# Kernel tuning notes

Hardware: AMD Instinct MI355X
Metric: run time of the kernel (lower is better)

The kernel has to match this reference:

```python
import math
import jax, jax.numpy as jnp
import numpy as np

B, N, D_IN = 8, 4096, 512  # batch, tokens (64x64 grid), d_inner = expand*d_model
MAX_DIFFUSION = 0.35
ALPHA_SCALE = 0.25
BETA_EPS = 1e-4


def setup_inputs() -> dict:
    key = jax.random.key(0)
    ks = jax.random.split(key, 6)
    x = jax.random.normal(ks[0], (B, N, D_IN), dtype=jnp.float32)
    # diffusion_gate: Linear(d_inner, d_inner) with tiny uniform init and softplus-inv(0.08) bias
    Wg = jax.random.uniform(ks[1], (D_IN, D_IN), jnp.float32, -1e-4, 1e-4)
    bg = jnp.full((D_IN,), math.log(math.exp(0.08) - 1.0), dtype=jnp.float32)
    log_base = jnp.full((1, D_IN), -2.5, dtype=jnp.float32)
    alpha_raw = 0.1 * jax.random.normal(ks[2], (1, 1, D_IN), dtype=jnp.float32)
    beta_raw = jnp.full((1, 1, D_IN), -2.0, dtype=jnp.float32)
    # out_complex: Linear(2*d_inner, d_inner, bias=False); torch weight shape [out, in]
    Wout = jax.random.normal(ks[3], (D_IN, 2 * D_IN), jnp.float32) / math.sqrt(2 * D_IN)
    Dparam = jnp.ones((D_IN,), dtype=jnp.float32)
    return {"x": x, "Wg": Wg, "bg": bg, "log_base": log_base,
            "alpha_raw": alpha_raw, "beta_raw": beta_raw,
            "Wout": Wout, "Dparam": Dparam, "k_steps": 4}


def _reaction(psi, alpha, beta, dt):
    # Exact update of q=|psi|^2 under dq/dt = 2*alpha*q - 2*beta*q^2; phase unchanged.
    eps = 1e-8
    q = jnp.real(psi) ** 2 + jnp.imag(psi) ** 2
    a = 2.0 * alpha
    b = 2.0 * beta
    exp_term = jnp.exp(-a * dt)
    denom = jnp.maximum(b * q + (a - b * q) * exp_term, eps)
    q_general = a * q / denom
    q_zero_alpha = q / (1.0 + b * q * dt)
    q_new = jnp.maximum(jnp.where(jnp.abs(a) < 1e-6, q_zero_alpha, q_general), 0.0)
    scale = jnp.sqrt(q_new / jnp.maximum(q, eps))
    return psi * scale


def reference(x, Wg, bg, log_base, alpha_raw, beta_raw, Wout, Dparam, k_steps):
    bsz, num_tokens, d_inner = x.shape
    h = w = int(math.isqrt(num_tokens))
    pooled = x.mean(axis=1)                                   # [B, d]
    gamma = jax.nn.softplus(pooled @ Wg.T + bg + log_base)    # [B, d]
    gamma = jnp.minimum(gamma, MAX_DIFFUSION).astype(jnp.float32)
    alpha = (ALPHA_SCALE * jnp.tanh(alpha_raw)).transpose(0, 2, 1)[..., None]   # [1, d, 1, 1]
    beta = (jax.nn.softplus(beta_raw) + BETA_EPS).transpose(0, 2, 1)[..., None]  # [1, d, 1, 1]
    # Periodic 2D Laplacian eigenvalues
    ky = jnp.arange(h, dtype=jnp.float32)
    kx = jnp.arange(w, dtype=jnp.float32)
    eig = (2.0 * jnp.cos(2.0 * jnp.pi * ky / h) - 2.0)[:, None] + \
          (2.0 * jnp.cos(2.0 * jnp.pi * kx / w) - 2.0)[None, :]  # [h, w]
    dt = 1.0 / max(int(k_steps), 1)
    psi = x.transpose(0, 2, 1).reshape(bsz, d_inner, h, w).astype(jnp.complex64)
    phase_arg = dt * gamma[:, :, None, None] * eig[None, None, :, :]  # [B, d, h, w]
    phase = jnp.cos(phase_arg) + 1j * jnp.sin(phase_arg)
    for _ in range(int(k_steps)):
        psi = _reaction(psi, alpha, beta, 0.5 * dt)
        psi = jnp.fft.ifft2(jnp.fft.fft2(psi, axes=(-2, -1)) * phase, axes=(-2, -1))
        psi = _reaction(psi, alpha, beta, 0.5 * dt)
    h_real = jnp.real(psi).reshape(bsz, d_inner, num_tokens).transpose(0, 2, 1)
    h_imag = jnp.imag(psi).reshape(bsz, d_inner, num_tokens).transpose(0, 2, 1)
    combined = jnp.concatenate([h_real, h_imag], axis=-1).astype(x.dtype)  # [B, N, 2d]
    return combined @ Wout.T + x * Dparam
```

## Files before the change

### kernel.cpp

```cpp
#include <hip/hip_runtime.h>
#include <math.h>


#define D_INNER 512
#define NTOK    4096

typedef _Float16 half8 __attribute__((ext_vector_type(8)));
typedef float    f32x4 __attribute__((ext_vector_type(4)));

struct cplx { float re, im; };

__device__ __forceinline__ cplx cmul(cplx a, cplx b) {
  return { a.re * b.re - a.im * b.im, a.re * b.im + a.im * b.re };
}

template<int CTRL>
__device__ __forceinline__ float dppf(float x) {
  return __int_as_float(__builtin_amdgcn_mov_dpp(__float_as_int(x), CTRL, 0xf, 0xf, true));
}
#define DPP_XOR1 0xB1
#define DPP_XOR2 0x4E

template<int SIGN>
__device__ __forceinline__ void fft16(cplx* a) {
  const float C16[8] = {1.f, 0.9238795325112867f, 0.7071067811865476f, 0.3826834323650898f,
                        0.f, -0.3826834323650898f, -0.7071067811865476f, -0.9238795325112867f};
  const float S16[8] = {0.f, 0.3826834323650898f, 0.7071067811865476f, 0.9238795325112867f,
                        1.f, 0.9238795325112867f, 0.7071067811865476f, 0.3826834323650898f};
  cplx t;
#define SWP(i, j) { t = a[i]; a[i] = a[j]; a[j] = t; }
  SWP(1, 8) SWP(2, 4) SWP(3, 12) SWP(5, 10) SWP(7, 14) SWP(11, 13)
#undef SWP
#pragma unroll
  for (int s = 1; s <= 4; ++s) {
    const int half = 1 << (s - 1);
#pragma unroll
    for (int base = 0; base < 16; base += (1 << s)) {
#pragma unroll
      for (int j = 0; j < (1 << (s - 1)); ++j) {
        const int ti = j << (4 - s);
        const float wc = C16[ti];
        const float ws = (SIGN < 0) ? -S16[ti] : S16[ti];
        cplx u = a[base + j];
        cplx v = a[base + j + half];
        cplx vw = { v.re * wc - v.im * ws, v.re * ws + v.im * wc };
        a[base + j]        = { u.re + vw.re, u.im + vw.im };
        a[base + j + half] = { u.re - vw.re, u.im - vw.im };
      }
    }
  }
}

__device__ __forceinline__ cplx fwd_cross(cplx z, bool s1, bool s2) {
  cplx w;  w.re = dppf<DPP_XOR2>(z.re);  w.im = dppf<DPP_XOR2>(z.im);
  cplx z1;
  z1.re = s2 ? (w.re - z.re) : (z.re + w.re);
  z1.im = s2 ? (w.im - z.im) : (z.im + w.im);
  cplx w2; w2.re = dppf<DPP_XOR1>(z1.re); w2.im = dppf<DPP_XOR1>(z1.im);
  cplx o;
  o.re = s1 ? (w2.re - (s2 ? z1.im : z1.re))
            : (z1.re + (s2 ? w2.im : w2.re));
  o.im = s1 ? (w2.im + (s2 ? z1.re : -z1.im))
            : (z1.im + (s2 ? -w2.re : w2.im));
  return o;
}

__device__ __forceinline__ cplx inv_cross(cplx z, bool s1, bool s2) {
  cplx w;  w.re = dppf<DPP_XOR1>(z.re);  w.im = dppf<DPP_XOR1>(z.im);
  cplx z1;
  z1.re = s1 ? (w.re - z.re) : (z.re + w.re);
  z1.im = s1 ? (w.im - z.im) : (z.im + w.im);
  cplx w2; w2.re = dppf<DPP_XOR2>(z1.re); w2.im = dppf<DPP_XOR2>(z1.im);
  cplx o;
  o.re = s2 ? (w2.re + (s1 ? z1.im : -z1.re))
            : (z1.re + (s1 ? -w2.im : w2.re));
  o.im = s2 ? (w2.im - (s1 ? z1.re : z1.im))
            : (z1.im + (s1 ? w2.re : w2.im));
  return o;
}

template<int SIGN>
__device__ __forceinline__ void fft64(cplx* a, bool s1, bool s2,
                                      const float* twc, const float* tws) {
  if (SIGN < 0) {
#pragma unroll
    for (int i = 0; i < 16; ++i) a[i] = fwd_cross(a[i], s1, s2);
#pragma unroll
    for (int i = 0; i < 16; ++i) {
      float c = twc[i], s = tws[i];
      cplx v = a[i];
      a[i] = { v.re * c + v.im * s, v.im * c - v.re * s };
    }
    fft16<-1>(a);
  } else {
    fft16<1>(a);
#pragma unroll
    for (int i = 0; i < 16; ++i) {
      float c = twc[i], s = tws[i];
      cplx v = a[i];
      a[i] = { v.re * c - v.im * s, v.im * c + v.re * s };
    }
#pragma unroll
    for (int i = 0; i < 16; ++i) a[i] = inv_cross(a[i], s1, s2);
  }
}

__device__ __forceinline__ void reaction_fast(cplx* a, float sA, float cB, float cC) {
#pragma unroll
  for (int i = 0; i < 16; ++i) {
    float q = fmaf(a[i].re, a[i].re, a[i].im * a[i].im);
    float s = sA * rsqrtf(fmaf(cB, q, cC));
    a[i].re *= s; a[i].im *= s;
  }
}


__global__ void zero_kernel(float* p, int n) {
  int i = blockIdx.x * blockDim.x + threadIdx.x;
  if (i < n) p[i] = 0.f;
}

__global__ __launch_bounds__(256) void transpose_pool_kernel(
    const float* __restrict__ x, float* __restrict__ xT, float* __restrict__ pooled) {
  __shared__ float tile[64][65];
  const int n0 = blockIdx.x * 64, d0 = blockIdx.y * 64, b = blockIdx.z;
  const int t = threadIdx.x;
  const int tc = t & 63, tr = t >> 6;
  const float* xp = x + ((size_t)b * NTOK + n0) * D_INNER + d0;
#pragma unroll
  for (int i = 0; i < 16; ++i) {
    int nl = tr + i * 4;
    tile[nl][tc] = xp[(size_t)nl * D_INNER + tc];
  }
  __syncthreads();
  float* xo = xT + ((size_t)b * D_INNER + d0) * NTOK + n0;
#pragma unroll
  for (int i = 0; i < 16; ++i) {
    int dl = tr + i * 4;
    xo[(size_t)dl * NTOK + tc] = tile[tc][dl];
  }
  if (t < 64) {
    float s = 0.f;
#pragma unroll
    for (int n = 0; n < 64; ++n) s += tile[n][t];
    atomicAdd(&pooled[b * D_INNER + d0 + t], s);
  }
}

__global__ __launch_bounds__(256) void gamma_kernel(
    const float* __restrict__ pooled, const float* __restrict__ Wg,
    const float* __restrict__ bg, const float* __restrict__ log_base,
    float* __restrict__ gamma) {
  int t = blockIdx.x * 256 + threadIdx.x;
  int b = t >> 9, j = t & 511;
  const float* pr = pooled + b * D_INNER;
  const float* wr = Wg + (size_t)j * D_INNER;
  float acc = 0.f;
#pragma unroll 4
  for (int d = 0; d < D_INNER; ++d) acc = fmaf(pr[d], wr[d], acc);
  float z = acc * (1.f / 4096.f) + bg[j] + log_base[j];
  float sp = fmaxf(z, 0.f) + log1pf(expf(-fabsf(z)));
  gamma[t] = fminf(sp, 0.35f);
}

__global__ __launch_bounds__(256) void plane_kernel(
    const float* __restrict__ xT, const float* __restrict__ gamma,
    const float* __restrict__ alpha_raw, const float* __restrict__ beta_raw,
    const int* __restrict__ kstep_p, _Float16* __restrict__ S) {
  __shared__ float2 T[64 * 65];
  __shared__ float2 P[64];
  const int blk = blockIdx.x;
  const int bb = blk >> 9, d = blk & 511;
  const int tid = threadIdx.x;
  const int lb = tid & 3;
  const int rr = tid >> 2;
  const bool s1 = lb & 1, s2 = (lb & 2) != 0;

  int ks = kstep_p[0]; if (ks < 1) ks = 1;
  const float dt  = 1.0f / (float)ks;
  const float dtr = 0.5f * dt;
  const float a2 = 2.0f * 0.25f * tanhf(alpha_raw[d]);
  float zb = beta_raw[d];
  const float b2 = 2.0f * (fmaxf(zb, 0.f) + log1pf(expf(-fabsf(zb))) + 1e-4f);

  _Float16* Sre = S + ((size_t)(bb * 1024 + d)) * NTOK + rr * 64 + lb * 16;
  _Float16* Sim = S + ((size_t)(bb * 1024 + 512 + d)) * NTOK + rr * 64 + lb * 16;

  if (a2 <= -1e-6f) {
    half8 z = {};
    *(half8*)&Sre[0] = z; *(half8*)&Sre[8] = z;
    *(half8*)&Sim[0] = z; *(half8*)&Sim[8] = z;
    return;
  }

  float sA, cB, cC;
  if (a2 < 1e-6f) {
    sA = 1.f; cB = b2 * dtr; cC = 1.f;
  } else {
    float ex = expf(-a2 * dtr);
    sA = sqrtf(a2); cB = b2 * (1.f - ex); cC = a2 * ex;
  }
  const float cg = dt * gamma[(bb << 9) + d];

  const float TWO_PI_64 = 6.283185307179586f / 64.0f;
  if (tid < 64) {
    float e = 2.0f * cosf(TWO_PI_64 * (float)tid) - 2.0f;
    float sv, cv; sincosf(cg * e, &sv, &cv);
    P[tid] = make_float2(cv * 0.015625f, sv * 0.015625f);
  }
  const int k2 = (lb == 1) ? 2 : ((lb == 2) ? 1 : lb);
  float twc[16], tws[16];
  {
    float c1, s1v; sincosf(TWO_PI_64 * (float)k2, &s1v, &c1);
    twc[0] = 1.f; tws[0] = 0.f;
#pragma unroll
    for (int i = 1; i < 16; ++i) {
      float pc = twc[i-1], ps = tws[i-1];
      twc[i] = pc * c1 - ps * s1v;
      tws[i] = ps * c1 + pc * s1v;
    }
  }

  cplx a[16];
  const float* px = xT + (size_t)blk * NTOK + rr * 64 + lb * 16;
#pragma unroll
  for (int i = 0; i < 4; ++i) {
    float4 v = *(const float4*)(px + i * 4);
    a[i*4+0] = { v.x, 0.f }; a[i*4+1] = { v.y, 0.f };
    a[i*4+2] = { v.z, 0.f }; a[i*4+3] = { v.w, 0.f };
  }
  __syncthreads();

  for (int step = 0; step < ks; ++step) {
    reaction_fast(a, sA, cB, cC);
    fft64<-1>(a, s1, s2, twc, tws);
    __syncthreads();
#pragma unroll
    for (int i = 0; i < 16; ++i)
      T[rr * 65 + (k2 + 4 * i)] = make_float2(a[i].re, a[i].im);
    __syncthreads();
#pragma unroll
    for (int i = 0; i < 16; ++i) {
      float2 v = T[(lb * 16 + i) * 65 + rr];
      a[i] = { v.x, v.y };
    }
    fft64<-1>(a, s1, s2, twc, tws);
    {
      float2 pc = P[rr];
      cplx pcc = { pc.x, pc.y };
#pragma unroll
      for (int i = 0; i < 16; ++i) {
        float2 pk = P[k2 + 4 * i];
        a[i] = cmul(a[i], cmul({pk.x, pk.y}, pcc));
      }
    }
    fft64<1>(a, s1, s2, twc, tws);
    __syncthreads();
#pragma unroll
    for (int i = 0; i < 16; ++i)
      T[(lb * 16 + i) * 65 + rr] = make_float2(a[i].re, a[i].im);
    __syncthreads();
#pragma unroll
    for (int i = 0; i < 16; ++i) {
      float2 v = T[rr * 65 + (k2 + 4 * i)];
      a[i] = { v.x, v.y };
    }
    fft64<1>(a, s1, s2, twc, tws);
    reaction_fast(a, sA, cB, cC);
  }

  half8 hr0, hr1, hi0, hi1;
#pragma unroll
  for (int i = 0; i < 8; ++i) {
    hr0[i] = (_Float16)a[i].re;     hi0[i] = (_Float16)a[i].im;
    hr1[i] = (_Float16)a[8+i].re;   hi1[i] = (_Float16)a[8+i].im;
  }
  *(half8*)&Sre[0] = hr0; *(half8*)&Sre[8] = hr1;
  *(half8*)&Sim[0] = hi0; *(half8*)&Sim[8] = hi1;
}

__global__ __launch_bounds__(256) void transpose_S_kernel(
    const _Float16* __restrict__ S, _Float16* __restrict__ ST) {
  __shared__ __attribute__((aligned(16))) _Float16 tile[64 * 64];
  const int n0 = blockIdx.x * 64, k0 = blockIdx.y * 64, b = blockIdx.z;
  const int t = threadIdx.x;
#pragma unroll
  for (int r = 0; r < 2; ++r) {
    int idx = r * 256 + t, kr = idx >> 3, c = idx & 7;
    half8 v = *(const half8*)&S[((size_t)b * 1024 + k0 + kr) * NTOK + n0 + c * 8];
    *(half8*)&tile[kr * 64 + ((c ^ (kr & 7)) * 8)] = v;
  }
  __syncthreads();
#pragma unroll
  for (int r = 0; r < 2; ++r) {
    int idx = r * 256 + t, nr = idx >> 3, ck = idx & 7;
    half8 v;
#pragma unroll
    for (int j = 0; j < 8; ++j) {
      int k = ck * 8 + j;
      v[j] = tile[k * 64 + (((nr >> 3) ^ (k & 7)) * 8) + (nr & 7)];
    }
    *(half8*)&ST[((size_t)b * NTOK + n0 + nr) * 1024 + k0 + ck * 8] = v;
  }
}

__global__ __launch_bounds__(256) void out_gemm_f16(
    const _Float16* __restrict__ ST, const float* __restrict__ Wout,
    const float* __restrict__ x, const float* __restrict__ Dp,
    float* __restrict__ out) {
  __shared__ __attribute__((aligned(16))) _Float16 Abuf[2][128 * 32];
  __shared__ __attribute__((aligned(16))) _Float16 Bbuf[2][128 * 32];
  const int t = threadIdx.x;
  const int n0 = blockIdx.x * 128, j0 = blockIdx.y * 128, b = blockIdx.z;
  const int w = t >> 6, l = t & 63;
  const int jw = (w & 1) * 64, nw = (w >> 1) * 64;
  const int l15 = l & 15, l4 = l >> 4;

  const int sr = t >> 1, skh = t & 1;
  const int br_ = t >> 2, bc = t & 3;
  const _Float16* Sb = ST + (size_t)b * NTOK * 1024;

  float aReg[16];
  half8 bReg0, bReg1;

  auto loadA = [&](int k0) {
    const float* src = Wout + (size_t)(j0 + sr) * 1024 + k0 + skh * 16;
    *(float4*)&aReg[0]  = *(const float4*)&src[0];
    *(float4*)&aReg[4]  = *(const float4*)&src[4];
    *(float4*)&aReg[8]  = *(const float4*)&src[8];
    *(float4*)&aReg[12] = *(const float4*)&src[12];
  };
  auto loadB = [&](int k0) {
    bReg0 = *(const half8*)&Sb[(size_t)(n0 + br_) * 1024 + k0 + bc * 8];
    bReg1 = *(const half8*)&Sb[(size_t)(n0 + 64 + br_) * 1024 + k0 + bc * 8];
  };
  auto writeA = [&](int buf) {
    half8 h0, h1;
#pragma unroll
    for (int i = 0; i < 8; ++i) { h0[i] = (_Float16)aReg[i]; h1[i] = (_Float16)aReg[8 + i]; }
    int c0 = skh * 2, c1 = skh * 2 + 1, s = (sr >> 1) & 3;
    *(half8*)&Abuf[buf][sr * 32 + ((c0 ^ s) * 8)] = h0;
    *(half8*)&Abuf[buf][sr * 32 + ((c1 ^ s) * 8)] = h1;
  };
  auto writeB = [&](int buf) {
    int r0 = br_, r1 = 64 + br_;
    *(half8*)&Bbuf[buf][r0 * 32 + ((bc ^ ((r0 >> 1) & 3)) * 8)] = bReg0;
    *(half8*)&Bbuf[buf][r1 * 32 + ((bc ^ ((r1 >> 1) & 3)) * 8)] = bReg1;
  };

  f32x4 acc[4][4] = {};
  loadA(0); loadB(0);
  writeA(0); writeB(0);
  __syncthreads();
  int cur = 0;
  for (int kt = 0; kt < 32; ++kt) {
    if (kt + 1 < 32) { loadA((kt + 1) * 32); loadB((kt + 1) * 32); }
    half8 af[4], bf[4];
#pragma unroll
    for (int ff = 0; ff < 4; ++ff) {
      int jr = jw + ff * 16 + l15;
      af[ff] = *(const half8*)&Abuf[cur][jr * 32 + (((l4 ^ (jr >> 1)) & 3) * 8)];
      int nr = nw + ff * 16 + l15;
      bf[ff] = *(const half8*)&Bbuf[cur][nr * 32 + (((l4 ^ (nr >> 1)) & 3) * 8)];
    }
#pragma unroll
    for (int jf = 0; jf < 4; ++jf)
#pragma unroll
      for (int nf = 0; nf < 4; ++nf)
        acc[jf][nf] = __builtin_amdgcn_mfma_f32_16x16x32_f16(af[jf], bf[nf], acc[jf][nf], 0, 0, 0);
    if (kt + 1 < 32) {
      cur ^= 1;
      writeA(cur); writeB(cur);
      __syncthreads();
    }
  }

#pragma unroll
  for (int jf = 0; jf < 4; ++jf) {
#pragma unroll
    for (int nf = 0; nf < 4; ++nf) {
      int jr4 = j0 + jw + jf * 16 + l4 * 4;
      int n   = n0 + nw + nf * 16 + l15;
      const float* xrow = x + ((size_t)b * NTOK + n) * D_INNER + jr4;
      float* orow = out + ((size_t)b * NTOK + n) * D_INNER + jr4;
      float4 xv = *(const float4*)xrow;
      float4 dv = *(const float4*)&Dp[jr4];
      float4 o;
      o.x = acc[jf][nf][0] + xv.x * dv.x;
      o.y = acc[jf][nf][1] + xv.y * dv.y;
      o.z = acc[jf][nf][2] + xv.z * dv.z;
      o.w = acc[jf][nf][3] + xv.w * dv.w;
      *(float4*)orow = o;
    }
  }
}


extern "C" void kernel_launch(void* const* d_in, const int* in_sizes, int n_in,
                              void* d_out, int out_size, void* d_ws, size_t ws_size,
                              hipStream_t stream) {
  const float* x         = (const float*)d_in[0];
  const float* Wg        = (const float*)d_in[1];
  const float* bg        = (const float*)d_in[2];
  const float* log_base  = (const float*)d_in[3];
  const float* alpha_raw = (const float*)d_in[4];
  const float* beta_raw  = (const float*)d_in[5];
  const float* Wout      = (const float*)d_in[6];
  const float* Dparam    = (const float*)d_in[7];
  const int*   kstep     = (const int*)d_in[8];
  float* out = (float*)d_out;

  char* ws = (char*)d_ws;
  float*    xT = (float*)ws;
  _Float16* S  = (_Float16*)(ws + 67108864);
  _Float16* STr = (_Float16*)ws;
  float* pooled = (float*)(ws + 134217728);
  float* gamma  = pooled + 8 * D_INNER;

  zero_kernel<<<16, 256, 0, stream>>>(pooled, 8 * D_INNER);
  transpose_pool_kernel<<<dim3(64, 8, 8), 256, 0, stream>>>(x, xT, pooled);
  gamma_kernel<<<16, 256, 0, stream>>>(pooled, Wg, bg, log_base, gamma);
  plane_kernel<<<4096, 256, 0, stream>>>(xT, gamma, alpha_raw, beta_raw, kstep, S);
  transpose_S_kernel<<<dim3(64, 16, 8), 256, 0, stream>>>(S, STr);
  out_gemm_f16<<<dim3(32, 4, 8), 256, 0, stream>>>(STr, Wout, x, Dparam, out);
}
```

Measured before the change: 505.3 us.

## Vectorize FFT math, merge reaction half-steps, pre-convert Wout, use global_load_lds

Rewrites the plane kernel's complex arithmetic with packed float2 vectors and branch-free cross-lane butterflies. Adjacent reaction half-steps are merged into one full-step update. A launch-bounds occupancy hint is added. Wout is converted to fp16 once in a separate kernel, and the GEMM stages A and B tiles straight into LDS with global_load_lds instead of going through registers; this drops the XOR swizzle, so LDS bank conflicts may rise.

Result: faster. 457.4 us (-9.5%).

```diff
diff --git a/kernel.cpp b/kernel.cpp
--- a/kernel.cpp
+++ b/kernel.cpp
@@ -7,27 +7,38 @@
 
 typedef _Float16 half8 __attribute__((ext_vector_type(8)));
 typedef float    f32x4 __attribute__((ext_vector_type(4)));
-
-struct cplx { float re, im; };
-
-__device__ __forceinline__ cplx cmul(cplx a, cplx b) {
-  return { a.re * b.re - a.im * b.im, a.re * b.im + a.im * b.re };
-}
+typedef float    f32x2 __attribute__((ext_vector_type(2)));
+
+#define DPP_XOR1 0xB1
+#define DPP_XOR2 0x4E
 
 template<int CTRL>
 __device__ __forceinline__ float dppf(float x) {
   return __int_as_float(__builtin_amdgcn_mov_dpp(__float_as_int(x), CTRL, 0xf, 0xf, true));
 }
-#define DPP_XOR1 0xB1
-#define DPP_XOR2 0x4E
+template<int CTRL>
+__device__ __forceinline__ f32x2 dpp2(f32x2 v) {
+  f32x2 r;
+  r.x = dppf<CTRL>(v.x);
+  r.y = dppf<CTRL>(v.y);
+  return r;
+}
+__device__ __forceinline__ f32x2 cswap(f32x2 v) { return __builtin_shufflevector(v, v, 1, 0); }
+
+__device__ __forceinline__ f32x2 cmulv(f32x2 a, f32x2 b) {
+  f32x2 ar = __builtin_shufflevector(a, a, 0, 0);
+  f32x2 ai = __builtin_shufflevector(a, a, 1, 1);
+  f32x2 bs = cswap(b) * (f32x2){-1.f, 1.f};
+  return ar * b + ai * bs;
+}
 
 template<int SIGN>
-__device__ __forceinline__ void fft16(cplx* a) {
+__device__ __forceinline__ void fft16v(f32x2* a) {
   const float C16[8] = {1.f, 0.9238795325112867f, 0.7071067811865476f, 0.3826834323650898f,
                         0.f, -0.3826834323650898f, -0.7071067811865476f, -0.9238795325112867f};
   const float S16[8] = {0.f, 0.3826834323650898f, 0.7071067811865476f, 0.9238795325112867f,
                         1.f, 0.9238795325112867f, 0.7071067811865476f, 0.3826834323650898f};
-  cplx t;
+  f32x2 t;
 #define SWP(i, j) { t = a[i]; a[i] = a[j]; a[j] = t; }
   SWP(1, 8) SWP(2, 4) SWP(3, 12) SWP(5, 10) SWP(7, 14) SWP(11, 13)
 #undef SWP
@@ -37,80 +48,66 @@
 #pragma unroll
     for (int base = 0; base < 16; base += (1 << s)) {
 #pragma unroll
-      for (int j = 0; j < (1 << (s - 1)); ++j) {
+      for (int j = 0; j < half; ++j) {
         const int ti = j << (4 - s);
         const float wc = C16[ti];
-        const float ws = (SIGN < 0) ? -S16[ti] : S16[ti];
-        cplx u = a[base + j];
-        cplx v = a[base + j + half];
-        cplx vw = { v.re * wc - v.im * ws, v.re * ws + v.im * wc };
-        a[base + j]        = { u.re + vw.re, u.im + vw.im };
-        a[base + j + half] = { u.re - vw.re, u.im - vw.im };
+        const float wsv = (SIGN < 0) ? -S16[ti] : S16[ti];
+        f32x2 u = a[base + j];
+        f32x2 v = a[base + j + half];
+        f32x2 vw = v * (f32x2){wc, wc} + cswap(v) * (f32x2){-wsv, wsv};
+        a[base + j]        = u + vw;
+        a[base + j + half] = u - vw;
       }
     }
   }
 }
 
-__device__ __forceinline__ cplx fwd_cross(cplx z, bool s1, bool s2) {
-  cplx w;  w.re = dppf<DPP_XOR2>(z.re);  w.im = dppf<DPP_XOR2>(z.im);
-  cplx z1;
-  z1.re = s2 ? (w.re - z.re) : (z.re + w.re);
-  z1.im = s2 ? (w.im - z.im) : (z.im + w.im);
-  cplx w2; w2.re = dppf<DPP_XOR1>(z1.re); w2.im = dppf<DPP_XOR1>(z1.im);
-  cplx o;
-  o.re = s1 ? (w2.re - (s2 ? z1.im : z1.re))
-            : (z1.re + (s2 ? w2.im : w2.re));
-  o.im = s1 ? (w2.im + (s2 ? z1.re : -z1.im))
-            : (z1.im + (s2 ? -w2.re : w2.im));
-  return o;
-}
-
-__device__ __forceinline__ cplx inv_cross(cplx z, bool s1, bool s2) {
-  cplx w;  w.re = dppf<DPP_XOR1>(z.re);  w.im = dppf<DPP_XOR1>(z.im);
-  cplx z1;
-  z1.re = s1 ? (w.re - z.re) : (z.re + w.re);
-  z1.im = s1 ? (w.im - z.im) : (z.im + w.im);
-  cplx w2; w2.re = dppf<DPP_XOR2>(z1.re); w2.im = dppf<DPP_XOR2>(z1.im);
-  cplx o;
-  o.re = s2 ? (w2.re + (s1 ? z1.im : -z1.re))
-            : (z1.re + (s1 ? -w2.im : w2.re));
-  o.im = s2 ? (w2.im - (s1 ? z1.re : z1.im))
-            : (z1.im + (s1 ? w2.re : w2.im));
-  return o;
-}
+template<int D1, int D2>
+__device__ __forceinline__ f32x2 cross4(f32x2 z, f32x2 sgn, f32x2 r, bool psel, bool qsw) {
+  f32x2 w  = dpp2<D1>(z);
+  f32x2 z1 = w + sgn * z;
+  f32x2 w2 = dpp2<D2>(z1);
+  f32x2 p  = psel ? w2 : z1;
+  f32x2 qb = psel ? z1 : w2;
+  f32x2 q  = qsw ? cswap(qb) : qb;
+  return p + q * r;
+}
+
+struct CrossCtl {
+  f32x2 sgnF, rF, sgnI, rI;
+  bool s1, s2;
+};
 
 template<int SIGN>
-__device__ __forceinline__ void fft64(cplx* a, bool s1, bool s2,
-                                      const float* twc, const float* tws) {
+__device__ __forceinline__ void fft64v(f32x2* a, const CrossCtl& c,
+                                       const float* twc, const float* tws) {
   if (SIGN < 0) {
 #pragma unroll
-    for (int i = 0; i < 16; ++i) a[i] = fwd_cross(a[i], s1, s2);
+    for (int i = 0; i < 16; ++i) a[i] = cross4<DPP_XOR2, DPP_XOR1>(a[i], c.sgnF, c.rF, c.s1, c.s2);
 #pragma unroll
     for (int i = 0; i < 16; ++i) {
-      float c = twc[i], s = tws[i];
-      cplx v = a[i];
-      a[i] = { v.re * c + v.im * s, v.im * c - v.re * s };
-    }
-    fft16<-1>(a);
+      float cc = twc[i], ss = tws[i];
+      a[i] = a[i] * (f32x2){cc, cc} + cswap(a[i]) * (f32x2){ss, -ss};
+    }
+    fft16v<-1>(a);
   } else {
-    fft16<1>(a);
+    fft16v<1>(a);
 #pragma unroll
     for (int i = 0; i < 16; ++i) {
-      float c = twc[i], s = tws[i];
-      cplx v = a[i];
-      a[i] = { v.re * c - v.im * s, v.im * c + v.re * s };
-    }
-#pragma unroll
-    for (int i = 0; i < 16; ++i) a[i] = inv_cross(a[i], s1, s2);
-  }
-}
-
-__device__ __forceinline__ void reaction_fast(cplx* a, float sA, float cB, float cC) {
+      float cc = twc[i], ss = tws[i];
+      a[i] = a[i] * (f32x2){cc, cc} + cswap(a[i]) * (f32x2){-ss, ss};
+    }
+#pragma unroll
+    for (int i = 0; i < 16; ++i) a[i] = cross4<DPP_XOR1, DPP_XOR2>(a[i], c.sgnI, c.rI, c.s2, c.s1);
+  }
+}
+
+__device__ __forceinline__ void reactv(f32x2* a, float sA, float cB, float cC) {
 #pragma unroll
   for (int i = 0; i < 16; ++i) {
-    float q = fmaf(a[i].re, a[i].re, a[i].im * a[i].im);
+    float q = fmaf(a[i].x, a[i].x, a[i].y * a[i].y);
     float s = sA * rsqrtf(fmaf(cB, q, cC));
-    a[i].re *= s; a[i].im *= s;
+    a[i] *= (f32x2){s, s};
   }
 }
 
@@ -118,6 +115,16 @@
 __global__ void zero_kernel(float* p, int n) {
   int i = blockIdx.x * blockDim.x + threadIdx.x;
   if (i < n) p[i] = 0.f;
+}
+
+__global__ __launch_bounds__(256) void convert_w_kernel(
+    const float* __restrict__ W, _Float16* __restrict__ Wh) {
+  int i = (blockIdx.x * 256 + threadIdx.x) * 8;
+  float4 v0 = *(const float4*)&W[i];
+  float4 v1 = *(const float4*)&W[i + 4];
+  half8 h = { (_Float16)v0.x, (_Float16)v0.y, (_Float16)v0.z, (_Float16)v0.w,
+              (_Float16)v1.x, (_Float16)v1.y, (_Float16)v1.z, (_Float16)v1.w };
+  *(half8*)&Wh[i] = h;
 }
 
 __global__ __launch_bounds__(256) void transpose_pool_kernel(
@@ -163,18 +170,17 @@
   gamma[t] = fminf(sp, 0.35f);
 }
 
-__global__ __launch_bounds__(256) void plane_kernel(
+__global__ __launch_bounds__(256, 4) void plane_kernel(
     const float* __restrict__ xT, const float* __restrict__ gamma,
     const float* __restrict__ alpha_raw, const float* __restrict__ beta_raw,
     const int* __restrict__ kstep_p, _Float16* __restrict__ S) {
-  __shared__ float2 T[64 * 65];
-  __shared__ float2 P[64];
+  __shared__ f32x2 T[64 * 65];
+  __shared__ f32x2 P[64];
   const int blk = blockIdx.x;
   const int bb = blk >> 9, d = blk & 511;
   const int tid = threadIdx.x;
   const int lb = tid & 3;
   const int rr = tid >> 2;
-  const bool s1 = lb & 1, s2 = (lb & 2) != 0;
 
   int ks = kstep_p[0]; if (ks < 1) ks = 1;
   const float dt  = 1.0f / (float)ks;
@@ -193,12 +199,16 @@
     return;
   }
 
-  float sA, cB, cC;
+  float sAh, cBh, cCh, sAf, cBf, cCf;
   if (a2 < 1e-6f) {
-    sA = 1.f; cB = b2 * dtr; cC = 1.f;
+    sAh = 1.f; cBh = b2 * dtr; cCh = 1.f;
+    sAf = 1.f; cBf = b2 * dt;  cCf = 1.f;
   } else {
-    float ex = expf(-a2 * dtr);
-    sA = sqrtf(a2); cB = b2 * (1.f - ex); cC = a2 * ex;
+    float exh = expf(-a2 * dtr);
+    float exf = exh * exh;
+    float sq = sqrtf(a2);
+    sAh = sq; cBh = b2 * (1.f - exh); cCh = a2 * exh;
+    sAf = sq; cBf = b2 * (1.f - exf); cCf = a2 * exf;
   }
   const float cg = dt * gamma[(bb << 9) + d];
 
@@ -206,9 +216,21 @@
   if (tid < 64) {
     float e = 2.0f * cosf(TWO_PI_64 * (float)tid) - 2.0f;
     float sv, cv; sincosf(cg * e, &sv, &cv);
-    P[tid] = make_float2(cv * 0.015625f, sv * 0.015625f);
+    P[tid] = (f32x2){cv * 0.015625f, sv * 0.015625f};
   }
   const int k2 = (lb == 1) ? 2 : ((lb == 2) ? 1 : lb);
+
+  CrossCtl ctl;
+  {
+    const bool s1 = lb & 1, s2 = (lb & 2) != 0;
+    const f32x2 ONE = {1.f, 1.f}, MONE = {-1.f, -1.f};
+    ctl.s1 = s1; ctl.s2 = s2;
+    ctl.sgnF = s2 ? MONE : ONE;
+    ctl.sgnI = s1 ? MONE : ONE;
+    ctl.rF = s2 ? (s1 ? (f32x2){-1.f, 1.f} : (f32x2){1.f, -1.f}) : (s1 ? MONE : ONE);
+    ctl.rI = s1 ? (s2 ? (f32x2){1.f, -1.f} : (f32x2){-1.f, 1.f}) : (s2 ? MONE : ONE);
+  }
+
   float twc[16], tws[16];
   {
     float c1, s1v; sincosf(TWO_PI_64 * (float)k2, &s1v, &c1);
@@ -221,59 +243,52 @@
     }
   }
 
-  cplx a[16];
+  f32x2 a[16];
   const float* px = xT + (size_t)blk * NTOK + rr * 64 + lb * 16;
 #pragma unroll
   for (int i = 0; i < 4; ++i) {
     float4 v = *(const float4*)(px + i * 4);
-    a[i*4+0] = { v.x, 0.f }; a[i*4+1] = { v.y, 0.f };
-    a[i*4+2] = { v.z, 0.f }; a[i*4+3] = { v.w, 0.f };
+    a[i*4+0] = (f32x2){v.x, 0.f}; a[i*4+1] = (f32x2){v.y, 0.f};
+    a[i*4+2] = (f32x2){v.z, 0.f}; a[i*4+3] = (f32x2){v.w, 0.f};
   }
   __syncthreads();
-
-  for (int step = 0; step < ks; ++step) {
-    reaction_fast(a, sA, cB, cC);
-    fft64<-1>(a, s1, s2, twc, tws);
+  const f32x2 pc = P[rr];
+
+  reactv(a, sAh, cBh, cCh);
+  for (int step = 0; ; ) {
+    fft64v<-1>(a, ctl, twc, tws);
     __syncthreads();
 #pragma unroll
     for (int i = 0; i < 16; ++i)
-      T[rr * 65 + (k2 + 4 * i)] = make_float2(a[i].re, a[i].im);
+      T[rr * 65 + (k2 + 4 * i)] = a[i];
     __syncthreads();
 #pragma unroll
-    for (int i = 0; i < 16; ++i) {
-      float2 v = T[(lb * 16 + i) * 65 + rr];
-      a[i] = { v.x, v.y };
-    }
-    fft64<-1>(a, s1, s2, twc, tws);
-    {
-      float2 pc = P[rr];
-      cplx pcc = { pc.x, pc.y };
-#pragma unroll
-      for (int i = 0; i < 16; ++i) {
-        float2 pk = P[k2 + 4 * i];
-        a[i] = cmul(a[i], cmul({pk.x, pk.y}, pcc));
-      }
-    }
-    fft64<1>(a, s1, s2, twc, tws);
+    for (int i = 0; i < 16; ++i)
+      a[i] = T[(lb * 16 + i) * 65 + rr];
+    fft64v<-1>(a, ctl, twc, tws);
+#pragma unroll
+    for (int i = 0; i < 16; ++i)
+      a[i] = cmulv(a[i], cmulv(P[k2 + 4 * i], pc));
+    fft64v<1>(a, ctl, twc, tws);
     __syncthreads();
 #pragma unroll
     for (int i = 0; i < 16; ++i)
-      T[(lb * 16 + i) * 65 + rr] = make_float2(a[i].re, a[i].im);
+      T[(lb * 16 + i) * 65 + rr] = a[i];
     __syncthreads();
 #pragma unroll
-    for (int i = 0; i < 16; ++i) {
-      float2 v = T[rr * 65 + (k2 + 4 * i)];
-      a[i] = { v.x, v.y };
-    }
-    fft64<1>(a, s1, s2, twc, tws);
-    reaction_fast(a, sA, cB, cC);
-  }
+    for (int i = 0; i < 16; ++i)
+      a[i] = T[rr * 65 + (k2 + 4 * i)];
+    fft64v<1>(a, ctl, twc, tws);
+    if (++step == ks) break;
+    reactv(a, sAf, cBf, cCf);
+  }
+  reactv(a, sAh, cBh, cCh);
 
   half8 hr0, hr1, hi0, hi1;
 #pragma unroll
   for (int i = 0; i < 8; ++i) {
-    hr0[i] = (_Float16)a[i].re;     hi0[i] = (_Float16)a[i].im;
-    hr1[i] = (_Float16)a[8+i].re;   hi1[i] = (_Float16)a[8+i].im;
+    hr0[i] = (_Float16)a[i].x;     hi0[i] = (_Float16)a[i].y;
+    hr1[i] = (_Float16)a[8+i].x;   hi1[i] = (_Float16)a[8+i].y;
   }
   *(half8*)&Sre[0] = hr0; *(half8*)&Sre[8] = hr1;
   *(half8*)&Sim[0] = hi0; *(half8*)&Sim[8] = hi1;
@@ -304,8 +319,12 @@
   }
 }
 
+#define GLDS16(g, l) __builtin_amdgcn_global_load_lds( \
+    (const __attribute__((address_space(1))) void*)(g), \
+    (__attribute__((address_space(3))) void*)(l), 16, 0, 0)
+
 __global__ __launch_bounds__(256) void out_gemm_f16(
-    const _Float16* __restrict__ ST, const float* __restrict__ Wout,
+    const _Float16* __restrict__ ST, const _Float16* __restrict__ Wh,
     const float* __restrict__ x, const float* __restrict__ Dp,
     float* __restrict__ out) {
   __shared__ __attribute__((aligned(16))) _Float16 Abuf[2][128 * 32];
@@ -316,63 +335,39 @@
   const int jw = (w & 1) * 64, nw = (w >> 1) * 64;
   const int l15 = l & 15, l4 = l >> 4;
 
-  const int sr = t >> 1, skh = t & 1;
-  const int br_ = t >> 2, bc = t & 3;
-  const _Float16* Sb = ST + (size_t)b * NTOK * 1024;
-
-  float aReg[16];
-  half8 bReg0, bReg1;
-
-  auto loadA = [&](int k0) {
-    const float* src = Wout + (size_t)(j0 + sr) * 1024 + k0 + skh * 16;
-    *(float4*)&aReg[0]  = *(const float4*)&src[0];
-    *(float4*)&aReg[4]  = *(const float4*)&src[4];
-    *(float4*)&aReg[8]  = *(const float4*)&src[8];
-    *(float4*)&aReg[12] = *(const float4*)&src[12];
+  const int rowg = w * 32 + (l >> 2);
+  const int colh = (l & 3) * 8;
+  const _Float16* gA0 = Wh + (size_t)(j0 + rowg) * 1024 + colh;
+  const _Float16* gB0 = ST + ((size_t)b * NTOK + n0 + rowg) * 1024 + colh;
+  const int lOff0 = rowg * 32 + colh, lOff1 = lOff0 + 16 * 32;
+
+  auto stage = [&](int buf, int kt) {
+    const int ko = kt * 32;
+    GLDS16(gA0 + ko,               &Abuf[buf][lOff0]);
+    GLDS16(gA0 + ko + 16 * 1024,   &Abuf[buf][lOff1]);
+    GLDS16(gB0 + ko,               &Bbuf[buf][lOff0]);
+    GLDS16(gB0 + ko + 16 * 1024,   &Bbuf[buf][lOff1]);
   };
-  auto loadB = [&](int k0) {
-    bReg0 = *(const half8*)&Sb[(size_t)(n0 + br_) * 1024 + k0 + bc * 8];
-    bReg1 = *(const half8*)&Sb[(size_t)(n0 + 64 + br_) * 1024 + k0 + bc * 8];
-  };
-  auto writeA = [&](int buf) {
-    half8 h0, h1;
-#pragma unroll
-    for (int i = 0; i < 8; ++i) { h0[i] = (_Float16)aReg[i]; h1[i] = (_Float16)aReg[8 + i]; }
-    int c0 = skh * 2, c1 = skh * 2 + 1, s = (sr >> 1) & 3;
-    *(half8*)&Abuf[buf][sr * 32 + ((c0 ^ s) * 8)] = h0;
-    *(half8*)&Abuf[buf][sr * 32 + ((c1 ^ s) * 8)] = h1;
-  };
-  auto writeB = [&](int buf) {
-    int r0 = br_, r1 = 64 + br_;
-    *(half8*)&Bbuf[buf][r0 * 32 + ((bc ^ ((r0 >> 1) & 3)) * 8)] = bReg0;
-    *(half8*)&Bbuf[buf][r1 * 32 + ((bc ^ ((r1 >> 1) & 3)) * 8)] = bReg1;
-  };
 
   f32x4 acc[4][4] = {};
-  loadA(0); loadB(0);
-  writeA(0); writeB(0);
+  stage(0, 0);
   __syncthreads();
   int cur = 0;
   for (int kt = 0; kt < 32; ++kt) {
-    if (kt + 1 < 32) { loadA((kt + 1) * 32); loadB((kt + 1) * 32); }
+    if (kt + 1 < 32) stage(cur ^ 1, kt + 1);
     half8 af[4], bf[4];
 #pragma unroll
     for (int ff = 0; ff < 4; ++ff) {
-      int jr = jw + ff * 16 + l15;
-      af[ff] = *(const half8*)&Abuf[cur][jr * 32 + (((l4 ^ (jr >> 1)) & 3) * 8)];
-      int nr = nw + ff * 16 + l15;
-      bf[ff] = *(const half8*)&Bbuf[cur][nr * 32 + (((l4 ^ (nr >> 1)) & 3) * 8)];
+      af[ff] = *(const half8*)&Abuf[cur][(jw + ff * 16 + l15) * 32 + l4 * 8];
+      bf[ff] = *(const half8*)&Bbuf[cur][(nw + ff * 16 + l15) * 32 + l4 * 8];
     }
 #pragma unroll
     for (int jf = 0; jf < 4; ++jf)
 #pragma unroll
       for (int nf = 0; nf < 4; ++nf)
         acc[jf][nf] = __builtin_amdgcn_mfma_f32_16x16x32_f16(af[jf], bf[nf], acc[jf][nf], 0, 0, 0);
-    if (kt + 1 < 32) {
-      cur ^= 1;
-      writeA(cur); writeB(cur);
-      __syncthreads();
-    }
+    __syncthreads();
+    cur ^= 1;
   }
 
 #pragma unroll
@@ -411,16 +406,18 @@
   float* out = (float*)d_out;
 
   char* ws = (char*)d_ws;
-  float*    xT = (float*)ws;
-  _Float16* S  = (_Float16*)(ws + 67108864);
+  float*    xT  = (float*)ws;
+  _Float16* S   = (_Float16*)(ws + 67108864);
   _Float16* STr = (_Float16*)ws;
   float* pooled = (float*)(ws + 134217728);
   float* gamma  = pooled + 8 * D_INNER;
+  _Float16* Wh  = (_Float16*)(ws + 134217728 + 65536);
 
   zero_kernel<<<16, 256, 0, stream>>>(pooled, 8 * D_INNER);
+  convert_w_kernel<<<256, 256, 0, stream>>>(Wout, Wh);
   transpose_pool_kernel<<<dim3(64, 8, 8), 256, 0, stream>>>(x, xT, pooled);
   gamma_kernel<<<16, 256, 0, stream>>>(pooled, Wg, bg, log_base, gamma);
   plane_kernel<<<4096, 256, 0, stream>>>(xT, gamma, alpha_raw, beta_raw, kstep, S);
   transpose_S_kernel<<<dim3(64, 16, 8), 256, 0, stream>>>(S, STr);
-  out_gemm_f16<<<dim3(32, 4, 8), 256, 0, stream>>>(STr, Wout, x, Dparam, out);
-}
+  out_gemm_f16<<<dim3(32, 4, 8), 256, 0, stream>>>(STr, Wh, x, Dparam, out);
+}
```
